# Performance work log

Measured on AMD Instinct MI355X. Metric: run time of the kernel, lower is better.

Reference implementation:

```python
import jax, jax.numpy as jnp
import numpy as np

EPS = 1e-12  # torch F.normalize eps


def conv1x1(x, W, b):
    # x: [B,C,H,W], W: [O,C], b: [O]
    return jnp.einsum('bchw,oc->bohw', x, W) + b[None, :, None, None]


def l2norm(x):
    n = jnp.linalg.norm(x, axis=-1, keepdims=True)
    return x / jnp.maximum(n, EPS)


def setup_inputs() -> dict:
    key = jax.random.key(0)
    ks = jax.random.split(key, 12)
    B, C, H, W = 8, 192, 128, 128
    heads = 8
    s = 1.0 / np.sqrt(C)
    return {
        'x1': jax.random.normal(ks[0], (B, C, H, W), jnp.float32),
        'x2': jax.random.normal(ks[1], (B, C, H, W), jnp.float32),
        'W_proj': jax.random.normal(ks[2], (C, C), jnp.float32) * s,
        'b_proj': jax.random.normal(ks[3], (C,), jnp.float32) * 0.01,
        'gate': jnp.ones((1,), jnp.float32),
        'pos_bias_h': jax.random.normal(ks[4], (1, heads, 1, 1), jnp.float32) * 0.01,
        'pos_bias_w': jax.random.normal(ks[5], (1, heads, 1, 1), jnp.float32) * 0.01,
        'W_m1': jax.random.normal(ks[6], (C, C), jnp.float32) * s,
        'b_m1': jax.random.normal(ks[7], (C,), jnp.float32) * 0.01,
        'W_m2': jax.random.normal(ks[8], (C, C), jnp.float32) * s,
        'b_m2': jax.random.normal(ks[9], (C,), jnp.float32) * 0.01,
    }


def reference(x1, x2, W_proj, b_proj, gate, pos_bias_h, pos_bias_w, W_m1, b_m1, W_m2, b_m2):
    temperature = 0.01
    num_heads = pos_bias_h.shape[1]
    B, C, h, w = x1.shape
    c = C // num_heads

    out1 = conv1x1(x1, W_proj, b_proj)
    out2 = conv1x1(x2, W_proj, b_proj)

    def to_h_tokens(o):  # 'b (head c) h w -> b head h (w c)'
        return o.reshape(B, num_heads, c, h, w).transpose(0, 1, 3, 4, 2).reshape(B, num_heads, h, w * c)

    def to_w_tokens(o):  # 'b (head c) h w -> b head w (h c)'
        return o.reshape(B, num_heads, c, h, w).transpose(0, 1, 4, 3, 2).reshape(B, num_heads, w, h * c)

    k1 = to_h_tokens(out1)
    v1 = k1
    k2 = to_w_tokens(out2)
    v2 = k2
    q2 = to_w_tokens(out1)
    q1 = to_h_tokens(out2)

    q1 = l2norm(q1); q2 = l2norm(q2)
    k1 = l2norm(k1); k2 = l2norm(k2)

    attn1 = jnp.einsum('bnid,bnjd->bnij', q1, k1) / temperature + pos_bias_h
    attn2 = jnp.einsum('bnid,bnjd->bnij', q2, k2) / temperature + pos_bias_w
    attn1 = jax.nn.softmax(attn1, axis=-1)
    attn2 = jax.nn.softmax(attn2, axis=-1)

    out3 = jnp.einsum('bnij,bnjd->bnid', attn1, v1) + q1  # [B,heads,h,w*c]
    out4 = jnp.einsum('bnij,bnjd->bnid', attn2, v2) + q2  # [B,heads,w,h*c]

    # 'b head h (w c) -> b (head c) h w'
    out3 = out3.reshape(B, num_heads, h, w, c).transpose(0, 1, 4, 2, 3).reshape(B, C, h, w)
    # 'b head w (h c) -> b (head c) h w'
    out4 = out4.reshape(B, num_heads, w, h, c).transpose(0, 1, 4, 3, 2).reshape(B, C, h, w)

    g = jax.nn.sigmoid(gate)[0]
    fusion = g * out3 + (1.0 - g) * out4
    out = conv1x1(fusion, W_proj, b_proj)
    out = conv1x1(jax.nn.gelu(conv1x1(out, W_m1, b_m1), approximate=False), W_m2, b_m2) + x1 + x2
    return out
```

## Files before the change

### kernel.cpp

```cpp
#include <hip/hip_runtime.h>
#include <math.h>


#define N_PIX 16384
#define W_DIM 128
#define C_DIM 192
#define C_PH  24
#define ELEMS 25165824
#define TINV  100.0f

typedef __bf16 bf16x8 __attribute__((ext_vector_type(8)));
typedef float  f32x4  __attribute__((ext_vector_type(4)));

__device__ __forceinline__ unsigned short f2bf(float f) {
    union { float f; unsigned u; } x; x.f = f;
    unsigned r = x.u + 0x7FFF + ((x.u >> 16) & 1);
    return (unsigned short)(r >> 16);
}
__device__ __forceinline__ float bf2f(unsigned short h) {
    union { unsigned u; float f; } x; x.u = ((unsigned)h) << 16; return x.f;
}
__device__ __forceinline__ unsigned pack2(unsigned short a, unsigned short b) {
    return (unsigned)a | ((unsigned)b << 16);
}

__global__ __launch_bounds__(256)
void conv_f32in(const float* __restrict__ X, const float* __restrict__ Wt,
                const float* __restrict__ bias, unsigned short* __restrict__ Y)
{
    __shared__ unsigned short Ah[64][40];
    __shared__ unsigned short Bh[256][40];

    const int tid = threadIdx.x;
    const int p0 = blockIdx.x << 8;
    const int m0 = blockIdx.y << 6;
    const int b  = blockIdx.z;
    const float* Xb = X + (size_t)b * C_DIM * N_PIX;

    const int wave = tid >> 6, lane = tid & 63;
    const int quad = lane >> 4, l16 = lane & 15;
    const int mw = (wave & 1) << 5;
    const int nw = (wave >> 1) << 7;
    const int koff = quad << 3;

    f32x4 acc[2][8];
    #pragma unroll
    for (int i = 0; i < 2; ++i)
        #pragma unroll
        for (int j = 0; j < 8; ++j) acc[i][j] = (f32x4){0.f, 0.f, 0.f, 0.f};

    for (int k0 = 0; k0 < C_DIM; k0 += 32) {
        #pragma unroll
        for (int i = 0; i < 2; ++i) {
            const int a = (tid << 1) + i;
            const int m = a >> 3, kq = a & 7;
            const float4 v = *(const float4*)(Wt + (size_t)(m0 + m) * C_DIM + k0 + (kq << 2));
            uint2 pk; pk.x = pack2(f2bf(v.x), f2bf(v.y)); pk.y = pack2(f2bf(v.z), f2bf(v.w));
            *(uint2*)(&Ah[m][kq << 2]) = pk;
        }
        #pragma unroll
        for (int r = 0; r < 2; ++r) {
            const int u = tid + (r << 8);
            const int kq = u & 7, p4 = (u >> 3) << 2;
            float4 f[4];
            #pragma unroll
            for (int i = 0; i < 4; ++i)
                f[i] = *(const float4*)(Xb + (size_t)(k0 + (kq << 2) + i) * N_PIX + p0 + p4);
            #pragma unroll
            for (int j = 0; j < 4; ++j) {
                uint2 pk;
                pk.x = pack2(f2bf((&f[0].x)[j]), f2bf((&f[1].x)[j]));
                pk.y = pack2(f2bf((&f[2].x)[j]), f2bf((&f[3].x)[j]));
                *(uint2*)(&Bh[p4 + j][kq << 2]) = pk;
            }
        }
        __syncthreads();

        bf16x8 af[2];
        #pragma unroll
        for (int mf = 0; mf < 2; ++mf)
            af[mf] = *(const bf16x8*)(&Ah[mw + (mf << 4) + l16][koff]);
        #pragma unroll
        for (int nf = 0; nf < 8; ++nf) {
            const bf16x8 bfr = *(const bf16x8*)(&Bh[nw + (nf << 4) + l16][koff]);
            #pragma unroll
            for (int mf = 0; mf < 2; ++mf)
                acc[mf][nf] = __builtin_amdgcn_mfma_f32_16x16x32_bf16(af[mf], bfr, acc[mf][nf], 0, 0, 0);
        }
        __syncthreads();
    }

    const size_t outb = (size_t)b * C_DIM * N_PIX;
    #pragma unroll
    for (int mf = 0; mf < 2; ++mf) {
        #pragma unroll
        for (int r = 0; r < 4; ++r) {
            const int m = m0 + mw + (mf << 4) + (quad << 2) + r;
            const float bm = bias[m];
            const size_t row = outb + (size_t)m * N_PIX;
            #pragma unroll
            for (int nf = 0; nf < 8; ++nf) {
                const int p = p0 + nw + (nf << 4) + l16;
                Y[row + p] = f2bf(acc[mf][nf][r] + bm);
            }
        }
    }
}

template<int MODE>
__global__ __launch_bounds__(256)
void conv_b16in(const unsigned short* __restrict__ X, const float* __restrict__ Wt,
                const float* __restrict__ bias, void* __restrict__ Yv,
                const float* __restrict__ R1, const float* __restrict__ R2)
{
    __shared__ unsigned short Ah[64][40];
    __shared__ unsigned short Bh[256][40];

    const int tid = threadIdx.x;
    const int p0 = blockIdx.x << 8;
    const int m0 = blockIdx.y << 6;
    const int b  = blockIdx.z;
    const unsigned short* Xb = X + (size_t)b * C_DIM * N_PIX;

    const int wave = tid >> 6, lane = tid & 63;
    const int quad = lane >> 4, l16 = lane & 15;
    const int mw = (wave & 1) << 5;
    const int nw = (wave >> 1) << 7;
    const int koff = quad << 3;

    f32x4 acc[2][8];
    #pragma unroll
    for (int i = 0; i < 2; ++i)
        #pragma unroll
        for (int j = 0; j < 8; ++j) acc[i][j] = (f32x4){0.f, 0.f, 0.f, 0.f};

    for (int k0 = 0; k0 < C_DIM; k0 += 32) {
        #pragma unroll
        for (int i = 0; i < 2; ++i) {
            const int a = (tid << 1) + i;
            const int m = a >> 3, kq = a & 7;
            const float4 v = *(const float4*)(Wt + (size_t)(m0 + m) * C_DIM + k0 + (kq << 2));
            uint2 pk; pk.x = pack2(f2bf(v.x), f2bf(v.y)); pk.y = pack2(f2bf(v.z), f2bf(v.w));
            *(uint2*)(&Ah[m][kq << 2]) = pk;
        }
        {
            const int kq = tid & 7, pg = (tid >> 3) << 3;
            uint4 f[4];
            #pragma unroll
            for (int i = 0; i < 4; ++i)
                f[i] = *(const uint4*)(Xb + (size_t)(k0 + (kq << 2) + i) * N_PIX + p0 + pg);
            #pragma unroll
            for (int j = 0; j < 8; ++j) {
                const unsigned short e0 = ((const unsigned short*)&f[0])[j];
                const unsigned short e1 = ((const unsigned short*)&f[1])[j];
                const unsigned short e2 = ((const unsigned short*)&f[2])[j];
                const unsigned short e3 = ((const unsigned short*)&f[3])[j];
                uint2 pk; pk.x = pack2(e0, e1); pk.y = pack2(e2, e3);
                *(uint2*)(&Bh[pg + j][kq << 2]) = pk;
            }
        }
        __syncthreads();

        bf16x8 af[2];
        #pragma unroll
        for (int mf = 0; mf < 2; ++mf)
            af[mf] = *(const bf16x8*)(&Ah[mw + (mf << 4) + l16][koff]);
        #pragma unroll
        for (int nf = 0; nf < 8; ++nf) {
            const bf16x8 bfr = *(const bf16x8*)(&Bh[nw + (nf << 4) + l16][koff]);
            #pragma unroll
            for (int mf = 0; mf < 2; ++mf)
                acc[mf][nf] = __builtin_amdgcn_mfma_f32_16x16x32_bf16(af[mf], bfr, acc[mf][nf], 0, 0, 0);
        }
        __syncthreads();
    }

    const size_t outb = (size_t)b * C_DIM * N_PIX;
    #pragma unroll
    for (int mf = 0; mf < 2; ++mf) {
        #pragma unroll
        for (int r = 0; r < 4; ++r) {
            const int m = m0 + mw + (mf << 4) + (quad << 2) + r;
            const float bm = bias[m];
            const size_t row = outb + (size_t)m * N_PIX;
            #pragma unroll
            for (int nf = 0; nf < 8; ++nf) {
                const int p = p0 + nw + (nf << 4) + l16;
                float v = acc[mf][nf][r] + bm;
                if (MODE == 1) v = 0.5f * v * (1.0f + erff(v * 0.70710678118654752f));
                if (MODE == 2) {
                    v += R1[row + p] + R2[row + p];
                    ((float*)Yv)[row + p] = v;
                } else {
                    ((unsigned short*)Yv)[row + p] = f2bf(v);
                }
            }
        }
    }
}

__global__ __launch_bounds__(256)
void norms_kernel(const unsigned short* __restrict__ o1,
                  const unsigned short* __restrict__ o2,
                  float* __restrict__ norms)
{
    __shared__ float hsum[128];
    __shared__ float wsum[128];
    const int tid = threadIdx.x;
    const int b = blockIdx.x, n = blockIdx.y;
    const int src = blockIdx.z >> 2, qt = blockIdx.z & 3;
    const unsigned short* basep = (src == 0 ? o1 : o2)
        + (size_t)b * C_DIM * N_PIX + (size_t)n * C_PH * N_PIX + (size_t)(qt * 6) * N_PIX;

    if (tid < 128) hsum[tid] = 0.0f;
    __syncthreads();

    const int tx = tid & 127, ty = tid >> 7;
    float accw = 0.0f;
    for (int hh = 0; hh < 64; ++hh) {
        const int h = (hh << 1) + ty;
        float rowacc = 0.0f;
        #pragma unroll
        for (int ch = 0; ch < 6; ++ch) {
            const float v = bf2f(basep[(size_t)ch * N_PIX + h * W_DIM + tx]);
            rowacc += v * v;
        }
        accw += rowacc;
        #pragma unroll
        for (int off = 32; off > 0; off >>= 1) rowacc += __shfl_down(rowacc, off);
        if ((tid & 63) == 0) atomicAdd(&hsum[h], rowacc);
    }
    if (ty == 0) wsum[tx] = accw;
    __syncthreads();
    if (ty == 1) wsum[tx] += accw;
    __syncthreads();

    float* np_ = norms + ((size_t)(src * 8 + b) * 8 + n) * 256;
    if (tid < 128) atomicAdd(&np_[tid], hsum[tid]);
    else           atomicAdd(&np_[tid], wsum[tid - 128]);
}

__global__ __launch_bounds__(256)
void scores_softmax(const unsigned short* __restrict__ o1,
                    const unsigned short* __restrict__ o2,
                    const float* __restrict__ norms, const float* __restrict__ gate,
                    unsigned short* __restrict__ P)
{
    __shared__ unsigned short Qh[64][40];
    __shared__ unsigned short Kh[128][40];
    __shared__ float rqv[64], rkv[128];

    const int tid = threadIdx.x;
    const int i0  = blockIdx.x << 6;
    const int bn  = blockIdx.y;
    const int dir = blockIdx.z;
    const int b = bn >> 3, n = bn & 7;

    const size_t base = (size_t)b * C_DIM * N_PIX + (size_t)n * C_PH * N_PIX;
    const unsigned short* Qb = (dir == 0 ? o2 : o1) + base;
    const unsigned short* Kb = (dir == 0 ? o1 : o2) + base;

    const int qsrc = (dir == 0) ? 1 : 0;
    const float* qn_g = norms + ((size_t)(qsrc * 8 + b) * 8 + n) * 256 + dir * 128;
    const float* kn_g = norms + ((size_t)((1 - qsrc) * 8 + b) * 8 + n) * 256 + dir * 128;

    if (tid < 64)        rqv[tid]      = TINV * rsqrtf(fmaxf(qn_g[i0 + tid], 1e-24f));
    else if (tid < 192)  rkv[tid - 64] = rsqrtf(fmaxf(kn_g[tid - 64], 1e-24f));

    const int wave = tid >> 6, lane = tid & 63;
    const int quad = lane >> 4, l16 = lane & 15;
    const int koff = quad << 3;

    f32x4 acc[8];
    #pragma unroll
    for (int j = 0; j < 8; ++j) acc[j] = (f32x4){0.f, 0.f, 0.f, 0.f};

    auto load_step = [&](int ks, uint4* pf) {
        const int ch = ks >> 2;
        const int x0 = (ks & 3) << 5;
        const size_t cb = (size_t)ch * N_PIX;
        if (dir == 0) {
            const int row = tid >> 2, q4 = tid & 3;
            pf[0] = *(const uint4*)(Qb + cb + (size_t)(i0 + row) * W_DIM + x0 + (q4 << 3));
            pf[1] = *(const uint4*)(Kb + cb + (size_t)row * W_DIM + x0 + (q4 << 3));
            pf[2] = *(const uint4*)(Kb + cb + (size_t)(64 + row) * W_DIM + x0 + (q4 << 3));
        } else {
            if (tid < 64) {
                const int wg = tid >> 3, kq = tid & 7;
                #pragma unroll
                for (int i = 0; i < 4; ++i)
                    pf[i] = *(const uint4*)(Qb + cb + (size_t)(x0 + (kq << 2) + i) * W_DIM + i0 + (wg << 3));
            } else if (tid < 192) {
                const int u = tid - 64;
                const int wg = u >> 3, kq = u & 7;
                #pragma unroll
                for (int i = 0; i < 4; ++i)
                    pf[i] = *(const uint4*)(Kb + cb + (size_t)(x0 + (kq << 2) + i) * W_DIM + (wg << 3));
            }
        }
    };
    auto store_step = [&](const uint4* pf) {
        if (dir == 0) {
            const int row = tid >> 2, q4 = tid & 3;
            *(uint4*)(&Qh[row][q4 << 3])      = pf[0];
            *(uint4*)(&Kh[row][q4 << 3])      = pf[1];
            *(uint4*)(&Kh[64 + row][q4 << 3]) = pf[2];
        } else {
            if (tid < 64) {
                const int wg = tid >> 3, kq = tid & 7;
                #pragma unroll
                for (int j = 0; j < 8; ++j) {
                    uint2 pk;
                    pk.x = pack2(((const unsigned short*)&pf[0])[j], ((const unsigned short*)&pf[1])[j]);
                    pk.y = pack2(((const unsigned short*)&pf[2])[j], ((const unsigned short*)&pf[3])[j]);
                    *(uint2*)(&Qh[(wg << 3) + j][kq << 2]) = pk;
                }
            } else if (tid < 192) {
                const int u = tid - 64;
                const int wg = u >> 3, kq = u & 7;
                #pragma unroll
                for (int j = 0; j < 8; ++j) {
                    uint2 pk;
                    pk.x = pack2(((const unsigned short*)&pf[0])[j], ((const unsigned short*)&pf[1])[j]);
                    pk.y = pack2(((const unsigned short*)&pf[2])[j], ((const unsigned short*)&pf[3])[j]);
                    *(uint2*)(&Kh[(wg << 3) + j][kq << 2]) = pk;
                }
            }
        }
    };
    auto compute_step = [&]() {
        const bf16x8 a = *(const bf16x8*)(&Qh[(wave << 4) + l16][koff]);
        #pragma unroll
        for (int nf = 0; nf < 8; ++nf) {
            const bf16x8 bfr = *(const bf16x8*)(&Kh[(nf << 4) + l16][koff]);
            acc[nf] = __builtin_amdgcn_mfma_f32_16x16x32_bf16(a, bfr, acc[nf], 0, 0, 0);
        }
    };

    uint4 pfA[4], pfB[4];
    load_step(0, pfA);
    for (int ks = 0; ks < 96; ks += 2) {
        store_step(pfA);
        __syncthreads();
        load_step(ks + 1, pfB);
        compute_step();
        __syncthreads();
        store_step(pfB);
        __syncthreads();
        if (ks + 2 < 96) load_step(ks + 2, pfA);
        compute_step();
        __syncthreads();
    }

    const float g = 1.0f / (1.0f + __expf(-gate[0]));
    const float gs = (dir == 0) ? g : (1.0f - g);
    unsigned short* Pg = P + (((size_t)dir * 64 + bn) << 14);

    #pragma unroll
    for (int r = 0; r < 4; ++r) {
        const int i_loc = (wave << 4) + (quad << 2) + r;
        const float rq = rqv[i_loc];
        float v[8], m = -1e30f;
        #pragma unroll
        for (int nf = 0; nf < 8; ++nf) {
            v[nf] = acc[nf][r] * rq * rkv[(nf << 4) + l16];
            m = fmaxf(m, v[nf]);
        }
        #pragma unroll
        for (int off = 1; off < 16; off <<= 1) m = fmaxf(m, __shfl_xor(m, off));
        float s = 0.0f;
        #pragma unroll
        for (int nf = 0; nf < 8; ++nf) { v[nf] = __expf(v[nf] - m); s += v[nf]; }
        #pragma unroll
        for (int off = 1; off < 16; off <<= 1) s += __shfl_xor(s, off);
        const float inv = gs / s;
        const size_t rowo = (size_t)(i0 + i_loc) * 128;
        #pragma unroll
        for (int nf = 0; nf < 8; ++nf)
            Pg[rowo + (nf << 4) + l16] = f2bf(v[nf] * inv);
    }
}

__global__ __launch_bounds__(256)
void pv_mfma(const unsigned short* __restrict__ o1, const unsigned short* __restrict__ o2,
             const unsigned short* __restrict__ P, const float* __restrict__ norms,
             const float* __restrict__ gate, unsigned short* __restrict__ fusion)
{
    __shared__ unsigned short P1s[128][40];
    __shared__ unsigned short A2s[128][40];
    __shared__ unsigned short P2s[128][40];
    __shared__ unsigned short A1Ts[128][40];
    __shared__ float rqs[256];

    const int tid = threadIdx.x;
    const int ch  = blockIdx.x;
    const int bn  = blockIdx.y;
    const int b = bn >> 3, n = bn & 7;

    const size_t pbase = (size_t)b * C_DIM * N_PIX + ((size_t)n * C_PH + ch) * N_PIX;
    const unsigned short* A1 = o1 + pbase;
    const unsigned short* A2 = o2 + pbase;
    const unsigned short* P1 = P + ((size_t)bn << 14);
    const unsigned short* P2 = P + ((size_t)(64 + bn) << 14);
    unsigned short* Fp = fusion + pbase;

    const float g = 1.0f / (1.0f + __expf(-gate[0]));
    if (tid < 128)
        rqs[tid] = g * rsqrtf(fmaxf(norms[(((size_t)8 + b) * 8 + n) * 256 + tid], 1e-24f));
    else
        rqs[tid] = (1.0f - g) * rsqrtf(fmaxf(norms[(((size_t)b) * 8 + n) * 256 + 128 + (tid - 128)], 1e-24f));

    const int wave = tid >> 6, lane = tid & 63;
    const int quad = lane >> 4, l16 = lane & 15;
    const int i0w = wave << 5;
    const int koff = quad << 3;

    f32x4 acc[2][8];
    #pragma unroll
    for (int i = 0; i < 2; ++i)
        #pragma unroll
        for (int j = 0; j < 8; ++j) acc[i][j] = (f32x4){0.f, 0.f, 0.f, 0.f};

    for (int k0 = 0; k0 < 128; k0 += 32) {
        #pragma unroll
        for (int r = 0; r < 2; ++r) {
            const int u = tid + (r << 8);
            const int row = u >> 2, k8 = u & 3;
            const size_t go = (size_t)row * 128 + k0 + (k8 << 3);
            *(uint4*)(&P1s[row][k8 << 3]) = *(const uint4*)(P1 + go);
            *(uint4*)(&A2s[row][k8 << 3]) = *(const uint4*)(A2 + go);
            *(uint4*)(&P2s[row][k8 << 3]) = *(const uint4*)(P2 + go);
        }
        if (tid < 128) {
            const int wg = tid >> 3, hq = tid & 7;
            uint4 f[4];
            #pragma unroll
            for (int i = 0; i < 4; ++i)
                f[i] = *(const uint4*)(A1 + (size_t)(k0 + (hq << 2) + i) * 128 + (wg << 3));
            #pragma unroll
            for (int j = 0; j < 8; ++j) {
                uint2 pk;
                pk.x = pack2(((const unsigned short*)&f[0])[j], ((const unsigned short*)&f[1])[j]);
                pk.y = pack2(((const unsigned short*)&f[2])[j], ((const unsigned short*)&f[3])[j]);
                *(uint2*)(&A1Ts[(wg << 3) + j][hq << 2]) = pk;
            }
        }
        __syncthreads();

        bf16x8 p1f[2], a2f[2];
        #pragma unroll
        for (int mf = 0; mf < 2; ++mf) {
            p1f[mf] = *(const bf16x8*)(&P1s[i0w + (mf << 4) + l16][koff]);
            a2f[mf] = *(const bf16x8*)(&A2s[i0w + (mf << 4) + l16][koff]);
        }
        #pragma unroll
        for (int nf = 0; nf < 8; ++nf) {
            const bf16x8 b1 = *(const bf16x8*)(&A1Ts[(nf << 4) + l16][koff]);
            const bf16x8 b2 = *(const bf16x8*)(&P2s[(nf << 4) + l16][koff]);
            #pragma unroll
            for (int mf = 0; mf < 2; ++mf) {
                acc[mf][nf] = __builtin_amdgcn_mfma_f32_16x16x32_bf16(p1f[mf], b1, acc[mf][nf], 0, 0, 0);
                acc[mf][nf] = __builtin_amdgcn_mfma_f32_16x16x32_bf16(a2f[mf], b2, acc[mf][nf], 0, 0, 0);
            }
        }
        __syncthreads();
    }

    #pragma unroll
    for (int mf = 0; mf < 2; ++mf) {
        #pragma unroll
        for (int r = 0; r < 4; ++r) {
            const int i = i0w + (mf << 4) + (quad << 2) + r;
            const float c1 = rqs[i];
            #pragma unroll
            for (int nf = 0; nf < 8; ++nf) {
                const int w = (nf << 4) + l16;
                const size_t o = (size_t)i * 128 + w;
                const float F = acc[mf][nf][r] + c1 * bf2f(A2[o]) + rqs[128 + w] * bf2f(A1[o]);
                Fp[o] = f2bf(F);
            }
        }
    }
}

extern "C" void kernel_launch(void* const* d_in, const int* in_sizes, int n_in,
                              void* d_out, int out_size, void* d_ws, size_t ws_size,
                              hipStream_t stream)
{
    (void)in_sizes; (void)n_in; (void)out_size; (void)ws_size;
    const float* x1     = (const float*)d_in[0];
    const float* x2     = (const float*)d_in[1];
    const float* W_proj = (const float*)d_in[2];
    const float* b_proj = (const float*)d_in[3];
    const float* gate   = (const float*)d_in[4];
    const float* W_m1   = (const float*)d_in[7];
    const float* b_m1   = (const float*)d_in[8];
    const float* W_m2   = (const float*)d_in[9];
    const float* b_m2   = (const float*)d_in[10];

    unsigned short* o1    = (unsigned short*)d_ws;
    unsigned short* o2    = o1 + ELEMS;
    float*          norms = (float*)(o2 + ELEMS);

    unsigned short* fusion = (unsigned short*)d_out;
    unsigned short* Pbuf   = fusion + ELEMS;

    const dim3 cgrid(64, 3, 8);
    conv_f32in<<<cgrid, 256, 0, stream>>>(x1, W_proj, b_proj, o1);
    conv_f32in<<<cgrid, 256, 0, stream>>>(x2, W_proj, b_proj, o2);

    hipMemsetAsync(norms, 0, 32768 * sizeof(float), stream);
    norms_kernel<<<dim3(8, 8, 8), 256, 0, stream>>>(o1, o2, norms);

    scores_softmax<<<dim3(2, 64, 2), 256, 0, stream>>>(o1, o2, norms, gate, Pbuf);
    pv_mfma<<<dim3(24, 64), 256, 0, stream>>>(o1, o2, Pbuf, norms, gate, fusion);

    conv_b16in<0><<<cgrid, 256, 0, stream>>>(fusion, W_proj, b_proj, o1, nullptr, nullptr);
    conv_b16in<1><<<cgrid, 256, 0, stream>>>(o1, W_m1, b_m1, o2, nullptr, nullptr);
    conv_b16in<2><<<cgrid, 256, 0, stream>>>(o2, W_m2, b_m2, d_out, x1, x2);
}
```

Measured before the change: 656.7 us.

## Precompute transposed activations and split-K the scores kernel across sixteen waves

The norms kernel becomes a transpose-plus-norms kernel that writes transposed copies of o1 and o2 while it computes the row and column sums of squares. The scores kernel now reads Q and K fragments straight from global memory, contiguous in both directions thanks to those copies. It also grows to 1024 threads, splitting the channel reduction four ways and summing partials through shared memory. The PV kernel loads the pre-transposed A1 with plain vector loads instead of transposing in registers. The cost is roughly 100 MB of extra transpose writes and moving Pbuf into the workspace, and the scores kernel now relies on global and cache loads with no LDS staging.

```diff
diff --git a/kernel.cpp b/kernel.cpp
--- a/kernel.cpp
+++ b/kernel.cpp
@@ -200,54 +200,90 @@
 }
 
 __global__ __launch_bounds__(256)
-void norms_kernel(const unsigned short* __restrict__ o1,
-                  const unsigned short* __restrict__ o2,
-                  float* __restrict__ norms)
+void transpose_norms(const unsigned short* __restrict__ o1,
+                     const unsigned short* __restrict__ o2,
+                     unsigned short* __restrict__ o1T,
+                     unsigned short* __restrict__ o2T,
+                     float* __restrict__ norms)
 {
-    __shared__ float hsum[128];
-    __shared__ float wsum[128];
+    __shared__ float hs[128];
+    __shared__ float wss[128];
+
     const int tid = threadIdx.x;
-    const int b = blockIdx.x, n = blockIdx.y;
-    const int src = blockIdx.z >> 2, qt = blockIdx.z & 3;
-    const unsigned short* basep = (src == 0 ? o1 : o2)
-        + (size_t)b * C_DIM * N_PIX + (size_t)n * C_PH * N_PIX + (size_t)(qt * 6) * N_PIX;
-
-    if (tid < 128) hsum[tid] = 0.0f;
+    const int ch  = blockIdx.x;
+    const int b   = blockIdx.y;
+    const int src = blockIdx.z;
+    const int n   = ch / 24;
+
+    const size_t poff = ((size_t)b * C_DIM + ch) * N_PIX;
+    const unsigned short* pin = (src ? o2 : o1) + poff;
+    unsigned short* pout      = (src ? o2T : o1T) + poff;
+
+    if (tid >= 128) wss[tid - 128] = 0.0f;
     __syncthreads();
 
-    const int tx = tid & 127, ty = tid >> 7;
-    float accw = 0.0f;
-    for (int hh = 0; hh < 64; ++hh) {
-        const int h = (hh << 1) + ty;
-        float rowacc = 0.0f;
-        #pragma unroll
-        for (int ch = 0; ch < 6; ++ch) {
-            const float v = bf2f(basep[(size_t)ch * N_PIX + h * W_DIM + tx]);
-            rowacc += v * v;
-        }
-        accw += rowacc;
-        #pragma unroll
-        for (int off = 32; off > 0; off >>= 1) rowacc += __shfl_down(rowacc, off);
-        if ((tid & 63) == 0) atomicAdd(&hsum[h], rowacc);
-    }
-    if (ty == 0) wsum[tx] = accw;
+    const int h0 = (tid >> 4) << 3;
+    const int w0 = (tid & 15) << 3;
+
+    uint4 r[8];
+    #pragma unroll
+    for (int i = 0; i < 8; ++i)
+        r[i] = *(const uint4*)(pin + (size_t)(h0 + i) * W_DIM + w0);
+
+    #pragma unroll
+    for (int j = 0; j < 8; ++j) {
+        uint4 o;
+        unsigned short* op = (unsigned short*)&o;
+        #pragma unroll
+        for (int i = 0; i < 8; ++i)
+            op[i] = ((const unsigned short*)&r[i])[j];
+        *(uint4*)(pout + (size_t)(w0 + j) * W_DIM + h0) = o;
+    }
+
+    float hp[8], wp[8];
+    #pragma unroll
+    for (int i = 0; i < 8; ++i) { hp[i] = 0.0f; wp[i] = 0.0f; }
+    #pragma unroll
+    for (int i = 0; i < 8; ++i) {
+        #pragma unroll
+        for (int j = 0; j < 8; ++j) {
+            const float v = bf2f(((const unsigned short*)&r[i])[j]);
+            hp[i] += v * v;
+            wp[j] += v * v;
+        }
+    }
+    #pragma unroll
+    for (int i = 0; i < 8; ++i) {
+        #pragma unroll
+        for (int off = 1; off < 16; off <<= 1) hp[i] += __shfl_xor(hp[i], off);
+    }
+    const int l16 = tid & 15;
+    if (l16 < 8) hs[h0 + l16] = hp[l16];
+    #pragma unroll
+    for (int j = 0; j < 8; ++j) {
+        wp[j] += __shfl_xor(wp[j], 16);
+        wp[j] += __shfl_xor(wp[j], 32);
+    }
+    if ((tid & 63) < 16) {
+        #pragma unroll
+        for (int j = 0; j < 8; ++j) atomicAdd(&wss[w0 + j], wp[j]);
+    }
     __syncthreads();
-    if (ty == 1) wsum[tx] += accw;
-    __syncthreads();
 
     float* np_ = norms + ((size_t)(src * 8 + b) * 8 + n) * 256;
-    if (tid < 128) atomicAdd(&np_[tid], hsum[tid]);
-    else           atomicAdd(&np_[tid], wsum[tid - 128]);
-}
-
-__global__ __launch_bounds__(256)
+    if (tid < 128) atomicAdd(&np_[tid], hs[tid]);
+    else           atomicAdd(&np_[tid], wss[tid - 128]);
+}
+
+__global__ __launch_bounds__(1024)
 void scores_softmax(const unsigned short* __restrict__ o1,
                     const unsigned short* __restrict__ o2,
+                    const unsigned short* __restrict__ o1T,
+                    const unsigned short* __restrict__ o2T,
                     const float* __restrict__ norms, const float* __restrict__ gate,
                     unsigned short* __restrict__ P)
 {
-    __shared__ unsigned short Qh[64][40];
-    __shared__ unsigned short Kh[128][40];
+    __shared__ float Sred[3][4][16][132];
     __shared__ float rqv[64], rkv[128];
 
     const int tid = threadIdx.x;
@@ -257,8 +293,8 @@
     const int b = bn >> 3, n = bn & 7;
 
     const size_t base = (size_t)b * C_DIM * N_PIX + (size_t)n * C_PH * N_PIX;
-    const unsigned short* Qb = (dir == 0 ? o2 : o1) + base;
-    const unsigned short* Kb = (dir == 0 ? o1 : o2) + base;
+    const unsigned short* Qb = (dir == 0 ? o2 : o1T) + base;
+    const unsigned short* Kb = (dir == 0 ? o1 : o2T) + base;
 
     const int qsrc = (dir == 0) ? 1 : 0;
     const float* qn_g = norms + ((size_t)(qsrc * 8 + b) * 8 + n) * 256 + dir * 128;
@@ -268,89 +304,42 @@
     else if (tid < 192)  rkv[tid - 64] = rsqrtf(fmaxf(kn_g[tid - 64], 1e-24f));
 
     const int wave = tid >> 6, lane = tid & 63;
+    const int iw = wave & 3;
+    const int kw = wave >> 2;
     const int quad = lane >> 4, l16 = lane & 15;
-    const int koff = quad << 3;
+
+    const unsigned short* rq = Qb + (size_t)(i0 + (iw << 4) + l16) * W_DIM + (quad << 3);
+    const unsigned short* rk = Kb + (size_t)l16 * W_DIM + (quad << 3);
 
     f32x4 acc[8];
     #pragma unroll
     for (int j = 0; j < 8; ++j) acc[j] = (f32x4){0.f, 0.f, 0.f, 0.f};
 
-    auto load_step = [&](int ks, uint4* pf) {
-        const int ch = ks >> 2;
-        const int x0 = (ks & 3) << 5;
-        const size_t cb = (size_t)ch * N_PIX;
-        if (dir == 0) {
-            const int row = tid >> 2, q4 = tid & 3;
-            pf[0] = *(const uint4*)(Qb + cb + (size_t)(i0 + row) * W_DIM + x0 + (q4 << 3));
-            pf[1] = *(const uint4*)(Kb + cb + (size_t)row * W_DIM + x0 + (q4 << 3));
-            pf[2] = *(const uint4*)(Kb + cb + (size_t)(64 + row) * W_DIM + x0 + (q4 << 3));
-        } else {
-            if (tid < 64) {
-                const int wg = tid >> 3, kq = tid & 7;
-                #pragma unroll
-                for (int i = 0; i < 4; ++i)
-                    pf[i] = *(const uint4*)(Qb + cb + (size_t)(x0 + (kq << 2) + i) * W_DIM + i0 + (wg << 3));
-            } else if (tid < 192) {
-                const int u = tid - 64;
-                const int wg = u >> 3, kq = u & 7;
-                #pragma unroll
-                for (int i = 0; i < 4; ++i)
-                    pf[i] = *(const uint4*)(Kb + cb + (size_t)(x0 + (kq << 2) + i) * W_DIM + (wg << 3));
-            }
-        }
-    };
-    auto store_step = [&](const uint4* pf) {
-        if (dir == 0) {
-            const int row = tid >> 2, q4 = tid & 3;
-            *(uint4*)(&Qh[row][q4 << 3])      = pf[0];
-            *(uint4*)(&Kh[row][q4 << 3])      = pf[1];
-            *(uint4*)(&Kh[64 + row][q4 << 3]) = pf[2];
-        } else {
-            if (tid < 64) {
-                const int wg = tid >> 3, kq = tid & 7;
-                #pragma unroll
-                for (int j = 0; j < 8; ++j) {
-                    uint2 pk;
-                    pk.x = pack2(((const unsigned short*)&pf[0])[j], ((const unsigned short*)&pf[1])[j]);
-                    pk.y = pack2(((const unsigned short*)&pf[2])[j], ((const unsigned short*)&pf[3])[j]);
-                    *(uint2*)(&Qh[(wg << 3) + j][kq << 2]) = pk;
-                }
-            } else if (tid < 192) {
-                const int u = tid - 64;
-                const int wg = u >> 3, kq = u & 7;
-                #pragma unroll
-                for (int j = 0; j < 8; ++j) {
-                    uint2 pk;
-                    pk.x = pack2(((const unsigned short*)&pf[0])[j], ((const unsigned short*)&pf[1])[j]);
-                    pk.y = pack2(((const unsigned short*)&pf[2])[j], ((const unsigned short*)&pf[3])[j]);
-                    *(uint2*)(&Kh[(wg << 3) + j][kq << 2]) = pk;
-                }
-            }
-        }
-    };
-    auto compute_step = [&]() {
-        const bf16x8 a = *(const bf16x8*)(&Qh[(wave << 4) + l16][koff]);
-        #pragma unroll
-        for (int nf = 0; nf < 8; ++nf) {
-            const bf16x8 bfr = *(const bf16x8*)(&Kh[(nf << 4) + l16][koff]);
-            acc[nf] = __builtin_amdgcn_mfma_f32_16x16x32_bf16(a, bfr, acc[nf], 0, 0, 0);
-        }
-    };
-
-    uint4 pfA[4], pfB[4];
-    load_step(0, pfA);
-    for (int ks = 0; ks < 96; ks += 2) {
-        store_step(pfA);
-        __syncthreads();
-        load_step(ks + 1, pfB);
-        compute_step();
-        __syncthreads();
-        store_step(pfB);
-        __syncthreads();
-        if (ks + 2 < 96) load_step(ks + 2, pfA);
-        compute_step();
-        __syncthreads();
-    }
+    #pragma unroll 2
+    for (int s = 0; s < 24; ++s) {
+        const int ks = kw * 24 + s;
+        const size_t off = (size_t)(ks >> 2) * N_PIX + (size_t)((ks & 3) << 5);
+        const uint4 qf = *(const uint4*)(rq + off);
+        uint4 kf[8];
+        #pragma unroll
+        for (int nf = 0; nf < 8; ++nf)
+            kf[nf] = *(const uint4*)(rk + off + (nf << 11));
+        const bf16x8 a = *(const bf16x8*)&qf;
+        #pragma unroll
+        for (int nf = 0; nf < 8; ++nf)
+            acc[nf] = __builtin_amdgcn_mfma_f32_16x16x32_bf16(a, *(const bf16x8*)&kf[nf], acc[nf], 0, 0, 0);
+    }
+
+    if (kw != 0) {
+        float* dst = &Sred[kw - 1][iw][0][0];
+        #pragma unroll
+        for (int nf = 0; nf < 8; ++nf)
+            #pragma unroll
+            for (int r = 0; r < 4; ++r)
+                dst[(size_t)((quad << 2) + r) * 132 + (nf << 4) + l16] = acc[nf][r];
+    }
+    __syncthreads();
+    if (kw != 0) return;
 
     const float g = 1.0f / (1.0f + __expf(-gate[0]));
     const float gs = (dir == 0) ? g : (1.0f - g);
@@ -358,12 +347,18 @@
 
     #pragma unroll
     for (int r = 0; r < 4; ++r) {
-        const int i_loc = (wave << 4) + (quad << 2) + r;
-        const float rq = rqv[i_loc];
+        const int row16 = (quad << 2) + r;
+        const int i_loc = (iw << 4) + row16;
+        const float rqs = rqv[i_loc];
         float v[8], m = -1e30f;
         #pragma unroll
         for (int nf = 0; nf < 8; ++nf) {
-            v[nf] = acc[nf][r] * rq * rkv[(nf << 4) + l16];
+            const int col = (nf << 4) + l16;
+            float sv = acc[nf][r]
+                     + Sred[0][iw][row16][col]
+                     + Sred[1][iw][row16][col]
+                     + Sred[2][iw][row16][col];
+            v[nf] = sv * rqs * rkv[col];
             m = fmaxf(m, v[nf]);
         }
         #pragma unroll
@@ -383,6 +378,7 @@
 
 __global__ __launch_bounds__(256)
 void pv_mfma(const unsigned short* __restrict__ o1, const unsigned short* __restrict__ o2,
+             const unsigned short* __restrict__ o1T,
              const unsigned short* __restrict__ P, const float* __restrict__ norms,
              const float* __restrict__ gate, unsigned short* __restrict__ fusion)
 {
@@ -398,8 +394,9 @@
     const int b = bn >> 3, n = bn & 7;
 
     const size_t pbase = (size_t)b * C_DIM * N_PIX + ((size_t)n * C_PH + ch) * N_PIX;
-    const unsigned short* A1 = o1 + pbase;
-    const unsigned short* A2 = o2 + pbase;
+    const unsigned short* A1  = o1 + pbase;
+    const unsigned short* A2  = o2 + pbase;
+    const unsigned short* A1T = o1T + pbase;
     const unsigned short* P1 = P + ((size_t)bn << 14);
     const unsigned short* P2 = P + ((size_t)(64 + bn) << 14);
     unsigned short* Fp = fusion + pbase;
@@ -427,23 +424,10 @@
             const int u = tid + (r << 8);
             const int row = u >> 2, k8 = u & 3;
             const size_t go = (size_t)row * 128 + k0 + (k8 << 3);
-            *(uint4*)(&P1s[row][k8 << 3]) = *(const uint4*)(P1 + go);
-            *(uint4*)(&A2s[row][k8 << 3]) = *(const uint4*)(A2 + go);
-            *(uint4*)(&P2s[row][k8 << 3]) = *(const uint4*)(P2 + go);
-        }
-        if (tid < 128) {
-            const int wg = tid >> 3, hq = tid & 7;
-            uint4 f[4];
-            #pragma unroll
-            for (int i = 0; i < 4; ++i)
-                f[i] = *(const uint4*)(A1 + (size_t)(k0 + (hq << 2) + i) * 128 + (wg << 3));
-            #pragma unroll
-            for (int j = 0; j < 8; ++j) {
-                uint2 pk;
-                pk.x = pack2(((const unsigned short*)&f[0])[j], ((const unsigned short*)&f[1])[j]);
-                pk.y = pack2(((const unsigned short*)&f[2])[j], ((const unsigned short*)&f[3])[j]);
-                *(uint2*)(&A1Ts[(wg << 3) + j][hq << 2]) = pk;
-            }
+            *(uint4*)(&P1s[row][k8 << 3])  = *(const uint4*)(P1 + go);
+            *(uint4*)(&A2s[row][k8 << 3])  = *(const uint4*)(A2 + go);
+            *(uint4*)(&P2s[row][k8 << 3])  = *(const uint4*)(P2 + go);
+            *(uint4*)(&A1Ts[row][k8 << 3]) = *(const uint4*)(A1T + go);
         }
         __syncthreads();
 
@@ -501,19 +485,21 @@
     unsigned short* o1    = (unsigned short*)d_ws;
     unsigned short* o2    = o1 + ELEMS;
     float*          norms = (float*)(o2 + ELEMS);
-
-    unsigned short* fusion = (unsigned short*)d_out;
-    unsigned short* Pbuf   = fusion + ELEMS;
+    unsigned short* Pbuf  = (unsigned short*)(norms + 32768);
+
+    unsigned short* o2T    = (unsigned short*)d_out;
+    unsigned short* fusion = o2T;
+    unsigned short* o1T    = o2T + ELEMS;
 
     const dim3 cgrid(64, 3, 8);
     conv_f32in<<<cgrid, 256, 0, stream>>>(x1, W_proj, b_proj, o1);
     conv_f32in<<<cgrid, 256, 0, stream>>>(x2, W_proj, b_proj, o2);
 
     hipMemsetAsync(norms, 0, 32768 * sizeof(float), stream);
-    norms_kernel<<<dim3(8, 8, 8), 256, 0, stream>>>(o1, o2, norms);
-
-    scores_softmax<<<dim3(2, 64, 2), 256, 0, stream>>>(o1, o2, norms, gate, Pbuf);
-    pv_mfma<<<dim3(24, 64), 256, 0, stream>>>(o1, o2, Pbuf, norms, gate, fusion);
+    transpose_norms<<<dim3(192, 8, 2), 256, 0, stream>>>(o1, o2, o1T, o2T, norms);
+
+    scores_softmax<<<dim3(2, 64, 2), 1024, 0, stream>>>(o1, o2, o1T, o2T, norms, gate, Pbuf);
+    pv_mfma<<<dim3(24, 64), 256, 0, stream>>>(o1, o2, o1T, Pbuf, norms, gate, fusion);
 
     conv_b16in<0><<<cgrid, 256, 0, stream>>>(fusion, W_proj, b_proj, o1, nullptr, nullptr);
     conv_b16in<1><<<cgrid, 256, 0, stream>>>(o1, W_m1, b_m1, o2, nullptr, nullptr);
```

Measured after the change: 635.3 us. 3.2% less time.
